# Performance work log

Hardware: AMD Instinct MI355X
Metric: run time of the kernel (lower is better)

Reference implementation:

```python
import jax, jax.numpy as jnp
import numpy as np

N_NODES = 100000
N_EDGES = 1600000
N_GRAPHS = 128
D = 108
IN_DIM = 146


def setup_inputs() -> dict:
    key = jax.random.key(0)
    ks = jax.random.split(key, 12)
    f32 = jnp.float32
    s = 0.05  # weight init scale
    inp = {}
    inp["nodes_feat"] = jax.random.normal(ks[0], (N_NODES, IN_DIM), f32)
    inp["snorm_n"] = jax.random.uniform(ks[1], (N_NODES, 1), f32)  # 1/sqrt(graph size) proxy
    inp["src"] = jax.random.randint(ks[2], (N_EDGES,), 0, N_NODES)
    inp["dst"] = jax.random.randint(ks[3], (N_EDGES,), 0, N_NODES)
    inp["graph_ids"] = jnp.sort(jax.random.randint(ks[4], (N_NODES,), 0, N_GRAPHS))
    inp["num_graphs"] = N_GRAPHS
    inp["W_emb"] = jax.random.normal(ks[5], (D, IN_DIM), f32) * s
    inp["b_emb"] = jnp.zeros((D,), f32)
    inp["W_pool"] = jax.random.normal(ks[6], (4, D, D), f32) * s
    inp["b_pool"] = jnp.zeros((4, D), f32)
    inp["W_node"] = jax.random.normal(ks[7], (4, D, 2 * D), f32) * s
    inp["b_node"] = jnp.zeros((4, D), f32)
    inp["W_r0"] = jax.random.normal(ks[8], (D // 2, D), f32) * s
    inp["b_r0"] = jnp.zeros((D // 2,), f32)
    inp["W_r1"] = jax.random.normal(ks[9], (D // 4, D // 2), f32) * s
    inp["b_r1"] = jnp.zeros((D // 4,), f32)
    inp["W_r2"] = jax.random.normal(ks[10], (10, D // 4), f32) * s
    inp["b_r2"] = jnp.zeros((10,), f32)
    return inp


def _forward(nodes_feat, snorm_n, W_emb, b_emb, W_pool, b_pool, W_node, b_node,
             W_r0, b_r0, W_r1, b_r1, W_r2, b_r2, src, dst, graph_ids, num_graphs):
    N = nodes_feat.shape[0]
    h = nodes_feat @ W_emb.T + b_emb  # [N, D] embedding_h
    # in-degree for mean aggregation (fixed over layers)
    deg = jax.ops.segment_sum(jnp.ones((src.shape[0],), h.dtype), dst, num_segments=N)
    deg = jnp.maximum(deg, 1.0)[:, None]
    n_layers = W_pool.shape[0]
    for l in range(n_layers):
        h_in = h
        # meanpool aggregator: relu(Linear(h_src)) then mean over in-neighbors
        pooled = jax.nn.relu(h @ W_pool[l].T + b_pool[l])  # [N, D]
        agg = jax.ops.segment_sum(pooled[src], dst, num_segments=N) / deg  # [N, D]
        # NodeApply: Linear(concat(h, c)) -> L2 normalize -> relu
        h = jnp.concatenate([h, agg], axis=1) @ W_node[l].T + b_node[l]
        h = h / jnp.maximum(jnp.linalg.norm(h, axis=1, keepdims=True), 1e-12)
        h = jax.nn.relu(h)
        h = h * snorm_n          # graph size normalization
        h = h_in + h             # residual
    # dgl.mean_nodes: per-graph mean readout
    cnt = jax.ops.segment_sum(jnp.ones((N,), h.dtype), graph_ids, num_segments=num_graphs)
    cnt = jnp.maximum(cnt, 1.0)[:, None]
    hg = jax.ops.segment_sum(h, graph_ids, num_segments=num_graphs) / cnt  # [G, D]
    # MLPReadout: D -> D/2 -> D/4 -> n_classes
    x = jax.nn.relu(hg @ W_r0.T + b_r0)
    x = jax.nn.relu(x @ W_r1.T + b_r1)
    return x @ W_r2.T + b_r2


def reference(nodes_feat, snorm_n, src, dst, graph_ids, num_graphs,
              W_emb, b_emb, W_pool, b_pool, W_node, b_node,
              W_r0, b_r0, W_r1, b_r1, W_r2, b_r2):
    return _forward(nodes_feat, snorm_n, W_emb, b_emb, W_pool, b_pool, W_node, b_node,
                    W_r0, b_r0, W_r1, b_r1, W_r2, b_r2, src, dst, graph_ids, num_graphs)
```

## Files before the change

### kernel.cpp

```cpp
#include <hip/hip_runtime.h>
#include <hip/hip_bf16.h>
#include <hip/hip_fp16.h>

#define N_NODES  100000
#define N_PAD    100096
#define N_EDGES  1600000
#define N_GRAPHS 128
#define D        108
#define IN_DIM   146
#define KP_H     128
#define KP_NF    160
#define PSTRIDE  128
#define NBUCKET  391
#define LBUF     8192

typedef _Float16 f16x8 __attribute__((ext_vector_type(8)));
typedef float    f32x4 __attribute__((ext_vector_type(4)));

__device__ __forceinline__ unsigned short f2h_bits(float v) {
  __half h = __float2half_rn(v);
  return __builtin_bit_cast(unsigned short, h);
}
__device__ __forceinline__ float h_bits2f(unsigned short u) {
  __half h = __builtin_bit_cast(__half, u);
  return __half2float(h);
}

__global__ __launch_bounds__(256)
void k_bhist(const int* __restrict__ dst, int* __restrict__ bhist) {
  __shared__ int bh[NBUCKET];
  int t = threadIdx.x;
  for (int i = t; i < NBUCKET; i += 256) bh[i] = 0;
  __syncthreads();
  int e0 = blockIdx.x * 2048;
#pragma unroll
  for (int j = 0; j < 8; j++) {
    int e = e0 + j * 256 + t;
    if (e < N_EDGES) atomicAdd(&bh[dst[e] >> 8], 1);
  }
  __syncthreads();
  for (int i = t; i < NBUCKET; i += 256)
    if (bh[i]) atomicAdd(&bhist[i], bh[i]);
}

__global__ __launch_bounds__(512)
void k_bscan(const int* __restrict__ bhist, int* __restrict__ boffs,
             int* __restrict__ bcur, int* __restrict__ offs) {
  __shared__ int sh[512];
  int t = threadIdx.x;
  sh[t] = (t < NBUCKET) ? bhist[t] : 0;
  __syncthreads();
  for (int off = 1; off < 512; off <<= 1) {
    int v = (t >= off) ? sh[t - off] : 0;
    __syncthreads();
    sh[t] += v;
    __syncthreads();
  }
  if (t < NBUCKET) {
    int excl = (t > 0) ? sh[t - 1] : 0;
    boffs[t] = excl;
    bcur[t]  = excl;
  }
  if (t == 0) { boffs[NBUCKET] = N_EDGES; offs[N_NODES] = N_EDGES; }
}

__global__ __launch_bounds__(256)
void k_binscatter(const int* __restrict__ src, const int* __restrict__ dst,
                  int* __restrict__ bcur, uint2* __restrict__ ebin) {
  __shared__ int lhist[NBUCKET];
  __shared__ int lbase[NBUCKET];
  int t = threadIdx.x;
  for (int i = t; i < NBUCKET; i += 256) lhist[i] = 0;
  __syncthreads();
  int e0 = blockIdx.x * 2048;
  int s[8], d[8], r[8];
#pragma unroll
  for (int j = 0; j < 8; j++) {
    int e = e0 + j * 256 + t;
    if (e < N_EDGES) {
      s[j] = src[e]; d[j] = dst[e];
      r[j] = atomicAdd(&lhist[d[j] >> 8], 1);
    }
  }
  __syncthreads();
  for (int i = t; i < NBUCKET; i += 256)
    lbase[i] = lhist[i] ? atomicAdd(&bcur[i], lhist[i]) : 0;
  __syncthreads();
#pragma unroll
  for (int j = 0; j < 8; j++) {
    int e = e0 + j * 256 + t;
    if (e < N_EDGES)
      ebin[(size_t)lbase[d[j] >> 8] + r[j]] = make_uint2((unsigned)s[j], (unsigned)d[j]);
  }
}

__global__ __launch_bounds__(256)
void k_scatter2(const uint2* __restrict__ ebin, const int* __restrict__ boffs,
                int* __restrict__ offs, int* __restrict__ esrc) {
  __shared__ int lcnt[256];
  __shared__ int lcur[256];
  __shared__ int lbuf[LBUF];
  int b = blockIdx.x;
  int t = threadIdx.x;
  int vbase = b << 8;
  int estart = boffs[b], eend = boffs[b + 1];
  int cnt = eend - estart;
  lcnt[t] = 0;
  __syncthreads();
  for (int e = estart + t; e < eend; e += 256)
    atomicAdd(&lcnt[ebin[e].y & 255], 1);
  __syncthreads();
  for (int off = 1; off < 256; off <<= 1) {
    int v = (t >= off) ? lcnt[t - off] : 0;
    __syncthreads();
    lcnt[t] += v;
    __syncthreads();
  }
  int excl = (t > 0) ? lcnt[t - 1] : 0;
  int v = vbase + t;
  if (v < N_NODES) offs[v] = estart + excl;
  lcur[t] = excl;
  __syncthreads();
  if (cnt <= LBUF) {
    for (int e = estart + t; e < eend; e += 256) {
      uint2 u = ebin[e];
      int pos = atomicAdd(&lcur[u.y & 255], 1);
      lbuf[pos] = (int)(u.x << 4);
    }
    __syncthreads();
    for (int i = t; i < cnt; i += 256) esrc[estart + i] = lbuf[i];
  } else {
    for (int e = estart + t; e < eend; e += 256) {
      uint2 u = ebin[e];
      int pos = atomicAdd(&lcur[u.y & 255], 1);
      esrc[estart + pos] = (int)(u.x << 4);
    }
  }
}

#define WEMB_OFF   0
#define WPOOL_OFF  17920
#define WNODE1_OFF (17920 + 4*14336)
#define WNODE2_OFF (17920 + 8*14336)
#define W_TOTAL    (17920 + 12*14336)

__global__ void k_split_w(const float* __restrict__ W_emb, const float* __restrict__ W_pool,
                          const float* __restrict__ W_node,
                          unsigned short* __restrict__ wF) {
  size_t stride = (size_t)gridDim.x * blockDim.x;
  for (size_t i = (size_t)blockIdx.x * blockDim.x + threadIdx.x; i < W_TOTAL; i += stride) {
    float v = 0.f;
    if (i < WPOOL_OFF) {
      int r = (int)(i / KP_NF), k = (int)(i % KP_NF);
      if (r < D && k < IN_DIM) v = W_emb[(size_t)r * IN_DIM + k];
    } else {
      size_t i2 = i - WPOOL_OFF;
      int seg = (int)(i2 / (4 * 14336));
      size_t r2 = i2 % (4 * 14336);
      int l = (int)(r2 / 14336);
      int n = (int)((r2 % 14336) / KP_H);
      int k = (int)(r2 % KP_H);
      if (n < D && k < D) {
        if (seg == 0)      v = W_pool[(size_t)l * D * D + (size_t)n * D + k];
        else if (seg == 1) v = W_node[(size_t)l * D * 2 * D + (size_t)n * 2 * D + k];
        else               v = W_node[(size_t)l * D * 2 * D + (size_t)n * 2 * D + D + k];
      }
    }
    wF[i] = f2h_bits(v);
  }
}

#define WS_STRIDE 76
__global__ __launch_bounds__(512)
void k_mm_embed(const float* __restrict__ Af,
                const unsigned short* __restrict__ W_,
                const float* __restrict__ bias,
                unsigned short* __restrict__ hF)
{
  __shared__ unsigned short Ws[112 * WS_STRIDE];

  const int t = threadIdx.x;
  const int lane = t & 63;
  const int wv = t >> 6;
  const int r15 = lane & 15;
  const int q = lane >> 4;
  const int m0 = blockIdx.x * 128 + wv * 16;
  const int row = m0 + r15;
  const bool rok = row < N_NODES;
  const float* rp_ = Af + (size_t)row * IN_DIM;

  f32x4 acc[7];
#pragma unroll
  for (int j = 0; j < 7; j++) acc[j] = f32x4{0.f, 0.f, 0.f, 0.f};

  for (int k0 = 0; k0 < KP_NF; k0 += 64) {
    const int klen = (KP_NF - k0 >= 64) ? 64 : (KP_NF - k0);
    const int ns = klen >> 5;
    __syncthreads();
    if (klen == 64) {
      for (int u = t; u < 896; u += 512) {
        int r_ = u >> 3, kq = u & 7;
        *(uint4*)&Ws[r_ * WS_STRIDE + kq * 8] =
            *(const uint4*)&W_[(size_t)r_ * KP_NF + k0 + kq * 8];
      }
    } else {
      for (int u = t; u < 448; u += 512) {
        int r_ = u >> 2, kq = u & 3;
        *(uint4*)&Ws[r_ * WS_STRIDE + kq * 8] =
            *(const uint4*)&W_[(size_t)r_ * KP_NF + k0 + kq * 8];
      }
    }
    f16x8 a[2];
#pragma unroll
    for (int s = 0; s < 2; s++) {
      if (s < ns) {
        int kb = k0 + s * 32 + q * 8;
        float vv[8];
        if (rok && kb + 8 <= IN_DIM) {
          const float2* pf = (const float2*)(rp_ + kb);
          float2 f0 = pf[0], f1 = pf[1], f2 = pf[2], f3 = pf[3];
          vv[0] = f0.x; vv[1] = f0.y; vv[2] = f1.x; vv[3] = f1.y;
          vv[4] = f2.x; vv[5] = f2.y; vv[6] = f3.x; vv[7] = f3.y;
        } else {
#pragma unroll
          for (int j = 0; j < 8; j++) {
            int k = kb + j;
            vv[j] = (rok && k < IN_DIM) ? rp_[k] : 0.f;
          }
        }
#pragma unroll
        for (int j = 0; j < 8; j++) a[s][j] = (_Float16)vv[j];
      }
    }
    __syncthreads();
#pragma unroll
    for (int s = 0; s < 2; s++) {
      if (s < ns) {
#pragma unroll
        for (int n = 0; n < 7; n++) {
          int wrow = n * 16 + r15;
          const f16x8 b = *(const f16x8*)&Ws[wrow * WS_STRIDE + s * 32 + q * 8];
          acc[n] = __builtin_amdgcn_mfma_f32_16x16x32_f16(a[s], b, acc[n], 0, 0, 0);
        }
      }
    }
  }

#pragma unroll
  for (int n = 0; n < 7; n++) {
    int col = n * 16 + r15;
    float bv = (col < D) ? bias[col] : 0.f;
#pragma unroll
    for (int r = 0; r < 4; r++) {
      int orow = m0 + q * 4 + r;
      float v = (orow < N_NODES && col < D) ? (acc[n][r] + bv) : 0.f;
      hF[(size_t)orow * KP_H + col] = f2h_bits(v);
    }
  }
  {
    int col = 112 + r15;
#pragma unroll
    for (int r = 0; r < 4; r++) {
      int orow = m0 + q * 4 + r;
      hF[(size_t)orow * KP_H + col] = 0;
    }
  }
}

__global__ __launch_bounds__(512)
void k_mm(const unsigned short* A1, int lda1, int K1,
          const unsigned short* __restrict__ W1, int ldw1,
          const unsigned short* A2, int lda2, int K2,
          const unsigned short* __restrict__ W2, int ldw2,
          const float* __restrict__ bias, int mode,
          __half* __restrict__ outH,
          unsigned short* hF,
          const float* __restrict__ snorm)
{
  __shared__ unsigned short Ws[112 * WS_STRIDE];

  const int t = threadIdx.x;
  const int lane = t & 63;
  const int wv = t >> 6;
  const int r15 = lane & 15;
  const int q = lane >> 4;
  const int m0 = blockIdx.x * 128 + wv * 16;

  f32x4 acc[7];
#pragma unroll
  for (int j = 0; j < 7; j++) acc[j] = f32x4{0.f, 0.f, 0.f, 0.f};

  auto do_seg = [&](const unsigned short* A, int lda, int K,
                    const unsigned short* W, int ldw) {
    for (int k0 = 0; k0 < K; k0 += 64) {
      const int klen = (K - k0 >= 64) ? 64 : (K - k0);
      __syncthreads();
      if (klen == 64) {
        for (int u = t; u < 896; u += 512) {
          int row = u >> 3, kq = u & 7;
          *(uint4*)&Ws[row * WS_STRIDE + kq * 8] =
              *(const uint4*)&W[(size_t)row * ldw + k0 + kq * 8];
        }
      } else {
        for (int u = t; u < 448; u += 512) {
          int row = u >> 2, kq = u & 3;
          *(uint4*)&Ws[row * WS_STRIDE + kq * 8] =
              *(const uint4*)&W[(size_t)row * ldw + k0 + kq * 8];
        }
      }
      f16x8 a[2];
      const int ns = klen >> 5;
#pragma unroll
      for (int s = 0; s < 2; s++) {
        if (s < ns) {
          size_t base = (size_t)(m0 + r15) * lda + k0 + s * 32 + q * 8;
          a[s] = *(const f16x8*)&A[base];
        }
      }
      __syncthreads();
#pragma unroll
      for (int s = 0; s < 2; s++) {
        if (s < ns) {
#pragma unroll
          for (int n = 0; n < 7; n++) {
            int wrow = n * 16 + r15;
            const f16x8 b = *(const f16x8*)&Ws[wrow * WS_STRIDE + s * 32 + q * 8];
            acc[n] = __builtin_amdgcn_mfma_f32_16x16x32_f16(a[s], b, acc[n], 0, 0, 0);
          }
        }
      }
    }
  };

  do_seg(A1, lda1, K1, W1, ldw1);
  if (A2) do_seg(A2, lda2, K2, W2, ldw2);

  if (mode == 2) {
    float ss[4] = {0.f, 0.f, 0.f, 0.f};
#pragma unroll
    for (int n = 0; n < 7; n++) {
      int col = n * 16 + r15;
      if (col < D) {
        float bv = bias[col];
#pragma unroll
        for (int r = 0; r < 4; r++) {
          float v = acc[n][r] + bv;
          ss[r] += v * v;
        }
      }
    }
#pragma unroll
    for (int m_ = 1; m_ <= 8; m_ <<= 1) {
#pragma unroll
      for (int r = 0; r < 4; r++) ss[r] += __shfl_xor(ss[r], m_, 64);
    }
    float inv[4], sn[4]; int rows[4];
#pragma unroll
    for (int r = 0; r < 4; r++) {
      rows[r] = m0 + q * 4 + r;
      float dn = fmaxf(sqrtf(ss[r]), 1e-12f);
      inv[r] = 1.0f / dn;
      sn[r] = (rows[r] < N_NODES) ? snorm[rows[r]] : 0.f;
    }
#pragma unroll
    for (int n = 0; n < 7; n++) {
      int col = n * 16 + r15;
      if (col >= D) continue;
      float bv = bias[col];
#pragma unroll
      for (int r = 0; r < 4; r++) {
        if (rows[r] >= N_NODES) continue;
        size_t idx = (size_t)rows[r] * KP_H + col;
        float hold = h_bits2f(hF[idx]);
        float v = acc[n][r] + bv;
        float x = fmaxf(v * inv[r], 0.f) * sn[r];
        hF[idx] = f2h_bits(hold + x);
      }
    }
  } else {
#pragma unroll
    for (int n = 0; n < 7; n++) {
      int col = n * 16 + r15;
      if (col >= D) continue;
      float bv = bias[col];
#pragma unroll
      for (int r = 0; r < 4; r++) {
        int row = m0 + q * 4 + r;
        if (row >= N_NODES) continue;
        float v = acc[n][r] + bv;
        outH[(size_t)row * PSTRIDE + col] = __float2half_rn(fmaxf(v, 0.f));
      }
    }
  }
}

__global__ __launch_bounds__(256)
void k_aggregate(const __half* __restrict__ pooled, const int* __restrict__ offsets,
                 const int* __restrict__ esrc,
                 unsigned int* __restrict__ aggF)
{
  int t = threadIdx.x;
  int lane = t & 63;
  int g = lane >> 4;
  int lp = lane & 15;
  int v = blockIdx.x * 4 + (t >> 6);
  if (v >= N_PAD) return;
  float va[8];
#pragma unroll
  for (int j = 0; j < 8; j++) va[j] = 0.f;
  int s0 = 0, s1 = 0;
  if (v < N_NODES) { s0 = offsets[v]; s1 = offsets[v + 1]; }
  const uint4* P = (const uint4*)pooled;
  int e = s0;
  for (; e + 15 < s1; e += 16) {
    unsigned o0 = (unsigned)esrc[e + g] + lp;
    unsigned o1 = (unsigned)esrc[e + 4 + g] + lp;
    unsigned o2 = (unsigned)esrc[e + 8 + g] + lp;
    unsigned o3 = (unsigned)esrc[e + 12 + g] + lp;
    uint4 u0 = P[o0];
    uint4 u1 = P[o1];
    uint4 u2 = P[o2];
    uint4 u3 = P[o3];
#pragma unroll
    for (int w = 0; w < 4; w++) {
      uint4 u = (w == 0) ? u0 : (w == 1) ? u1 : (w == 2) ? u2 : u3;
      float2 f0 = __half22float2(__builtin_bit_cast(__half2, u.x));
      float2 f1 = __half22float2(__builtin_bit_cast(__half2, u.y));
      float2 f2 = __half22float2(__builtin_bit_cast(__half2, u.z));
      float2 f3 = __half22float2(__builtin_bit_cast(__half2, u.w));
      va[0] += f0.x; va[1] += f0.y; va[2] += f1.x; va[3] += f1.y;
      va[4] += f2.x; va[5] += f2.y; va[6] += f3.x; va[7] += f3.y;
    }
  }
  for (; e + 7 < s1; e += 8) {
    unsigned o0 = (unsigned)esrc[e + g] + lp;
    unsigned o1 = (unsigned)esrc[e + 4 + g] + lp;
    uint4 u0 = P[o0];
    uint4 u1 = P[o1];
#pragma unroll
    for (int w = 0; w < 2; w++) {
      uint4 u = (w == 0) ? u0 : u1;
      float2 f0 = __half22float2(__builtin_bit_cast(__half2, u.x));
      float2 f1 = __half22float2(__builtin_bit_cast(__half2, u.y));
      float2 f2 = __half22float2(__builtin_bit_cast(__half2, u.z));
      float2 f3 = __half22float2(__builtin_bit_cast(__half2, u.w));
      va[0] += f0.x; va[1] += f0.y; va[2] += f1.x; va[3] += f1.y;
      va[4] += f2.x; va[5] += f2.y; va[6] += f3.x; va[7] += f3.y;
    }
  }
  for (; e < s1; e += 4) {
    int idx = e + g;
    if (idx < s1) {
      unsigned o = (unsigned)esrc[idx] + lp;
      uint4 u = P[o];
      float2 f0 = __half22float2(__builtin_bit_cast(__half2, u.x));
      float2 f1 = __half22float2(__builtin_bit_cast(__half2, u.y));
      float2 f2 = __half22float2(__builtin_bit_cast(__half2, u.z));
      float2 f3 = __half22float2(__builtin_bit_cast(__half2, u.w));
      va[0] += f0.x; va[1] += f0.y; va[2] += f1.x; va[3] += f1.y;
      va[4] += f2.x; va[5] += f2.y; va[6] += f3.x; va[7] += f3.y;
    }
  }
#pragma unroll
  for (int j = 0; j < 8; j++) {
    va[j] += __shfl_xor(va[j], 16, 64);
    va[j] += __shfl_xor(va[j], 32, 64);
  }
  if (g == 0) {
    int dgi = s1 - s0; if (dgi < 1) dgi = 1;
    float inv = 1.0f / (float)dgi;
    unsigned int w_[4];
#pragma unroll
    for (int p = 0; p < 4; p++) {
      unsigned short h0 = f2h_bits(va[2 * p] * inv);
      unsigned short h1 = f2h_bits(va[2 * p + 1] * inv);
      w_[p] = (unsigned)h0 | ((unsigned)h1 << 16);
    }
    *(uint4*)&aggF[(size_t)v * 64 + lp * 4] = make_uint4(w_[0], w_[1], w_[2], w_[3]);
  }
}

__global__ __launch_bounds__(256)
void k_gm_part(const unsigned short* __restrict__ hF,
               const int* __restrict__ gid, float* __restrict__ hgpart) {
  int g = blockIdx.x >> 3;
  int j = blockIdx.x & 7;
  int t = threadIdx.x;
  int c = t & 127, rp = t >> 7;
  int lo = 0, hi = N_NODES;
  while (lo < hi) { int m = (lo + hi) >> 1; if (gid[m] < g) lo = m + 1; else hi = m; }
  int s = lo;
  hi = N_NODES;
  while (lo < hi) { int m = (lo + hi) >> 1; if (gid[m] < g + 1) lo = m + 1; else hi = m; }
  int e = lo;
  int per = ((e - s) + 7) >> 3;
  int vs = s + j * per;
  int ve = vs + per; if (ve > e) ve = e;
  float acc = 0.f;
  if (c < D) {
    for (int v = vs + rp; v < ve; v += 2) {
      acc += h_bits2f(hF[(size_t)v * KP_H + c]);
    }
  }
  __shared__ float part[2][128];
  part[rp][c] = acc;
  __syncthreads();
  if (rp == 0 && c < D)
    hgpart[(size_t)blockIdx.x * D + c] = part[0][c] + part[1][c];
}

__global__ __launch_bounds__(128)
void k_gm_fin(const float* __restrict__ hgpart, const int* __restrict__ gid,
              float* __restrict__ hg) {
  int g = blockIdx.x;
  int t = threadIdx.x;
  int lo = 0, hi = N_NODES;
  while (lo < hi) { int m = (lo + hi) >> 1; if (gid[m] < g) lo = m + 1; else hi = m; }
  int s = lo;
  hi = N_NODES;
  while (lo < hi) { int m = (lo + hi) >> 1; if (gid[m] < g + 1) lo = m + 1; else hi = m; }
  int cnt = lo - s; if (cnt < 1) cnt = 1;
  if (t < D) {
    float sum = 0.f;
#pragma unroll
    for (int j = 0; j < 8; j++) sum += hgpart[(size_t)(g * 8 + j) * D + t];
    hg[g * D + t] = sum / (float)cnt;
  }
}

__global__ __launch_bounds__(64)
void k_readout(const float* __restrict__ hg,
               const float* __restrict__ Wr0, const float* __restrict__ br0,
               const float* __restrict__ Wr1, const float* __restrict__ br1,
               const float* __restrict__ Wr2, const float* __restrict__ br2,
               float* __restrict__ out) {
  int g = blockIdx.x;
  int t = threadIdx.x;
  __shared__ float x0[D];
  __shared__ float x1[54];
  __shared__ float x2[27];
  for (int i = t; i < D; i += 64) x0[i] = hg[g * D + i];
  __syncthreads();
  if (t < 54) {
    float v = br0[t];
    for (int k = 0; k < D; k++) v += x0[k] * Wr0[t * D + k];
    x1[t] = fmaxf(v, 0.f);
  }
  __syncthreads();
  if (t < 27) {
    float v = br1[t];
    for (int k = 0; k < 54; k++) v += x1[k] * Wr1[t * 54 + k];
    x2[t] = fmaxf(v, 0.f);
  }
  __syncthreads();
  if (t < 10) {
    float v = br2[t];
    for (int k = 0; k < 27; k++) v += x2[k] * Wr2[t * 27 + k];
    out[g * 10 + t] = v;
  }
}

extern "C" void kernel_launch(void* const* d_in, const int* in_sizes, int n_in,
                              void* d_out, int out_size, void* d_ws, size_t ws_size,
                              hipStream_t stream) {
  const float* nodes_feat = (const float*)d_in[0];
  const float* snorm_n    = (const float*)d_in[1];
  const int*   src        = (const int*)d_in[2];
  const int*   dst        = (const int*)d_in[3];
  const int*   gid        = (const int*)d_in[4];
  const float* W_emb      = (const float*)d_in[6];
  const float* b_emb      = (const float*)d_in[7];
  const float* W_pool     = (const float*)d_in[8];
  const float* b_pool     = (const float*)d_in[9];
  const float* W_node     = (const float*)d_in[10];
  const float* b_node     = (const float*)d_in[11];
  const float* W_r0       = (const float*)d_in[12];
  const float* b_r0       = (const float*)d_in[13];
  const float* W_r1       = (const float*)d_in[14];
  const float* b_r1       = (const float*)d_in[15];
  const float* W_r2       = (const float*)d_in[16];
  const float* b_r2       = (const float*)d_in[17];
  float* out = (float*)d_out;

  char* ws = (char*)d_ws;
  size_t off = 0;
  auto alloc = [&](size_t bytes) { size_t o = off; off = (off + bytes + 255) & ~(size_t)255; return o; };

  __half* buf1 = (__half*)(ws + alloc((size_t)N_NODES * PSTRIDE * 2));
  unsigned short* hF   = (unsigned short*)(ws + alloc((size_t)N_PAD * KP_H * 2));
  unsigned short* aggF = (unsigned short*)(ws + alloc((size_t)N_PAD * KP_H * 2));
  uint2* ebin = (uint2*)(ws + alloc((size_t)N_EDGES * 8));
  int* esrc  = (int*)(ws + alloc((size_t)N_EDGES * 4));
  int* offs  = (int*)(ws + alloc((size_t)(N_NODES + 1) * 4));
  int* bhist = (int*)(ws + alloc((size_t)(NBUCKET + 1) * 4));
  int* boffs = (int*)(ws + alloc((size_t)(NBUCKET + 1) * 4));
  int* bcur  = (int*)(ws + alloc((size_t)(NBUCKET + 1) * 4));
  unsigned short* wF = (unsigned short*)(ws + alloc((size_t)W_TOTAL * 2));
  float* hgpart = (float*)(ws + alloc((size_t)N_GRAPHS * 8 * D * 4));
  float* hg = (float*)(ws + alloc((size_t)N_GRAPHS * D * 4));
  (void)ws_size; (void)n_in; (void)in_sizes; (void)out_size;

  hipMemsetAsync(bhist, 0, (size_t)NBUCKET * 4, stream);

  k_split_w<<<(W_TOTAL + 255) / 256, 256, 0, stream>>>(W_emb, W_pool, W_node, wF);

  const int EB = (N_EDGES + 2047) / 2048;
  k_bhist<<<EB, 256, 0, stream>>>(dst, bhist);
  k_bscan<<<1, 512, 0, stream>>>(bhist, boffs, bcur, offs);
  k_binscatter<<<EB, 256, 0, stream>>>(src, dst, bcur, ebin);
  k_scatter2<<<NBUCKET, 256, 0, stream>>>(ebin, boffs, offs, esrc);

  const int GEMM_GRID = N_PAD / 128;
  k_mm_embed<<<GEMM_GRID, 512, 0, stream>>>(nodes_feat, wF + WEMB_OFF, b_emb, hF);

  for (int l = 0; l < 4; l++) {
    const unsigned short* wp  = wF + WPOOL_OFF  + (size_t)l * 14336;
    const unsigned short* wn1 = wF + WNODE1_OFF + (size_t)l * 14336;
    const unsigned short* wn2 = wF + WNODE2_OFF + (size_t)l * 14336;
    const float* bp = b_pool + (size_t)l * D;
    const float* bn = b_node + (size_t)l * D;

    k_mm<<<GEMM_GRID, 512, 0, stream>>>(hF, KP_H, KP_H,
                                        wp, KP_H,
                                        nullptr, 0, 0, nullptr, 0,
                                        bp, 1, buf1, nullptr, nullptr);
    k_aggregate<<<N_PAD / 4, 256, 0, stream>>>(buf1, offs, esrc, (unsigned int*)aggF);
    k_mm<<<GEMM_GRID, 512, 0, stream>>>(hF, KP_H, KP_H,
                                        wn1, KP_H,
                                        aggF, KP_H, KP_H,
                                        wn2, KP_H,
                                        bn, 2, nullptr, hF, snorm_n);
  }

  k_gm_part<<<N_GRAPHS * 8, 256, 0, stream>>>(hF, gid, hgpart);
  k_gm_fin<<<N_GRAPHS, 128, 0, stream>>>(hgpart, gid, hg);
  k_readout<<<N_GRAPHS, 64, 0, stream>>>(hg, W_r0, b_r0, W_r1, b_r1, W_r2, b_r2, out);
}
```

Baseline: 566.0 us.

## Double-buffer weight tiles in LDS for embed and layer GEMM kernels

Both GEMM kernels now keep two LDS buffers for the weight chunk. The next chunk is staged while MFMAs run on the current one, leaving one barrier per chunk instead of two. The layer GEMM also merges its two K segments into one chunk loop and assumes K is a multiple of 64. This doubles LDS use per block, which may lower occupancy, and the win is limited because the weights are small and cached.

```diff
diff --git a/kernel.cpp b/kernel.cpp
--- a/kernel.cpp
+++ b/kernel.cpp
@@ -177,7 +177,7 @@
                 const float* __restrict__ bias,
                 unsigned short* __restrict__ hF)
 {
-  __shared__ unsigned short Ws[112 * WS_STRIDE];
+  __shared__ unsigned short Ws[2][112 * WS_STRIDE];
 
   const int t = threadIdx.x;
   const int lane = t & 63;
@@ -193,23 +193,29 @@
 #pragma unroll
   for (int j = 0; j < 7; j++) acc[j] = f32x4{0.f, 0.f, 0.f, 0.f};
 
-  for (int k0 = 0; k0 < KP_NF; k0 += 64) {
-    const int klen = (KP_NF - k0 >= 64) ? 64 : (KP_NF - k0);
-    const int ns = klen >> 5;
-    __syncthreads();
+  const int NCH = 3;
+  auto stage = [&](int buf, int k0, int klen) {
     if (klen == 64) {
       for (int u = t; u < 896; u += 512) {
         int r_ = u >> 3, kq = u & 7;
-        *(uint4*)&Ws[r_ * WS_STRIDE + kq * 8] =
+        *(uint4*)&Ws[buf][r_ * WS_STRIDE + kq * 8] =
             *(const uint4*)&W_[(size_t)r_ * KP_NF + k0 + kq * 8];
       }
     } else {
       for (int u = t; u < 448; u += 512) {
         int r_ = u >> 2, kq = u & 3;
-        *(uint4*)&Ws[r_ * WS_STRIDE + kq * 8] =
+        *(uint4*)&Ws[buf][r_ * WS_STRIDE + kq * 8] =
             *(const uint4*)&W_[(size_t)r_ * KP_NF + k0 + kq * 8];
       }
     }
+  };
+
+  stage(0, 0, 64);
+  __syncthreads();
+  for (int c = 0; c < NCH; c++) {
+    const int k0 = c * 64;
+    const int klen = (KP_NF - k0 >= 64) ? 64 : (KP_NF - k0);
+    const int ns = klen >> 5;
     f16x8 a[2];
 #pragma unroll
     for (int s = 0; s < 2; s++) {
@@ -232,18 +238,22 @@
         for (int j = 0; j < 8; j++) a[s][j] = (_Float16)vv[j];
       }
     }
-    __syncthreads();
+    if (c + 1 < NCH) {
+      int nk0 = (c + 1) * 64;
+      stage((c + 1) & 1, nk0, (KP_NF - nk0 >= 64) ? 64 : (KP_NF - nk0));
+    }
 #pragma unroll
     for (int s = 0; s < 2; s++) {
       if (s < ns) {
 #pragma unroll
         for (int n = 0; n < 7; n++) {
           int wrow = n * 16 + r15;
-          const f16x8 b = *(const f16x8*)&Ws[wrow * WS_STRIDE + s * 32 + q * 8];
+          const f16x8 b = *(const f16x8*)&Ws[c & 1][wrow * WS_STRIDE + s * 32 + q * 8];
           acc[n] = __builtin_amdgcn_mfma_f32_16x16x32_f16(a[s], b, acc[n], 0, 0, 0);
         }
       }
     }
+    __syncthreads();
   }
 
 #pragma unroll
@@ -277,7 +287,7 @@
           unsigned short* hF,
           const float* __restrict__ snorm)
 {
-  __shared__ unsigned short Ws[112 * WS_STRIDE];
+  __shared__ unsigned short Ws[2][112 * WS_STRIDE];
 
   const int t = threadIdx.x;
   const int lane = t & 63;
@@ -286,54 +296,52 @@
   const int q = lane >> 4;
   const int m0 = blockIdx.x * 128 + wv * 16;
 
+  const int nch1 = K1 >> 6;
+  const int nch2 = A2 ? (K2 >> 6) : 0;
+  const int ncht = nch1 + nch2;
+
   f32x4 acc[7];
 #pragma unroll
   for (int j = 0; j < 7; j++) acc[j] = f32x4{0.f, 0.f, 0.f, 0.f};
 
-  auto do_seg = [&](const unsigned short* A, int lda, int K,
-                    const unsigned short* W, int ldw) {
-    for (int k0 = 0; k0 < K; k0 += 64) {
-      const int klen = (K - k0 >= 64) ? 64 : (K - k0);
-      __syncthreads();
-      if (klen == 64) {
-        for (int u = t; u < 896; u += 512) {
-          int row = u >> 3, kq = u & 7;
-          *(uint4*)&Ws[row * WS_STRIDE + kq * 8] =
-              *(const uint4*)&W[(size_t)row * ldw + k0 + kq * 8];
-        }
-      } else {
-        for (int u = t; u < 448; u += 512) {
-          int row = u >> 2, kq = u & 3;
-          *(uint4*)&Ws[row * WS_STRIDE + kq * 8] =
-              *(const uint4*)&W[(size_t)row * ldw + k0 + kq * 8];
-        }
-      }
-      f16x8 a[2];
-      const int ns = klen >> 5;
-#pragma unroll
-      for (int s = 0; s < 2; s++) {
-        if (s < ns) {
-          size_t base = (size_t)(m0 + r15) * lda + k0 + s * 32 + q * 8;
-          a[s] = *(const f16x8*)&A[base];
-        }
-      }
-      __syncthreads();
-#pragma unroll
-      for (int s = 0; s < 2; s++) {
-        if (s < ns) {
-#pragma unroll
-          for (int n = 0; n < 7; n++) {
-            int wrow = n * 16 + r15;
-            const f16x8 b = *(const f16x8*)&Ws[wrow * WS_STRIDE + s * 32 + q * 8];
-            acc[n] = __builtin_amdgcn_mfma_f32_16x16x32_f16(a[s], b, acc[n], 0, 0, 0);
-          }
-        }
-      }
-    }
+  auto chunk_W = [&](int c, const unsigned short*& W, int& ldw, int& k0) {
+    if (c < nch1) { W = W1; ldw = ldw1; k0 = c << 6; }
+    else          { W = W2; ldw = ldw2; k0 = (c - nch1) << 6; }
   };
-
-  do_seg(A1, lda1, K1, W1, ldw1);
-  if (A2) do_seg(A2, lda2, K2, W2, ldw2);
+  auto stage = [&](int buf, int c) {
+    const unsigned short* W; int ldw, k0;
+    chunk_W(c, W, ldw, k0);
+    for (int u = t; u < 896; u += 512) {
+      int row = u >> 3, kq = u & 7;
+      *(uint4*)&Ws[buf][row * WS_STRIDE + kq * 8] =
+          *(const uint4*)&W[(size_t)row * ldw + k0 + kq * 8];
+    }
+  };
+
+  stage(0, 0);
+  __syncthreads();
+  for (int c = 0; c < ncht; c++) {
+    const unsigned short* A; int lda, k0;
+    if (c < nch1) { A = A1; lda = lda1; k0 = c << 6; }
+    else          { A = A2; lda = lda2; k0 = (c - nch1) << 6; }
+    f16x8 a[2];
+#pragma unroll
+    for (int s = 0; s < 2; s++) {
+      size_t base = (size_t)(m0 + r15) * lda + k0 + s * 32 + q * 8;
+      a[s] = *(const f16x8*)&A[base];
+    }
+    if (c + 1 < ncht) stage((c + 1) & 1, c + 1);
+#pragma unroll
+    for (int s = 0; s < 2; s++) {
+#pragma unroll
+      for (int n = 0; n < 7; n++) {
+        int wrow = n * 16 + r15;
+        const f16x8 b = *(const f16x8*)&Ws[c & 1][wrow * WS_STRIDE + s * 32 + q * 8];
+        acc[n] = __builtin_amdgcn_mfma_f32_16x16x32_f16(a[s], b, acc[n], 0, 0, 0);
+      }
+    }
+    __syncthreads();
+  }
 
   if (mode == 2) {
     float ss[4] = {0.f, 0.f, 0.f, 0.f};
```

New measurement: 528.4 us. 6.7% less time.
